# Performance work log

Hardware: AMD Instinct MI355X
Metric: run time of the kernel (lower is better)

Reference implementation:

```python
import jax, jax.numpy as jnp
import numpy as np

B, S, D, H = 4, 2048, 1024, 16
DH = D // H
SCALE = float(np.sqrt(DH))


def setup_inputs() -> dict:
    key = jax.random.key(0)
    ks = jax.random.split(key, 5)
    std = 1.0 / np.sqrt(D)
    return {
        "x": jax.random.normal(ks[0], (B, S, D), dtype=jnp.float32),
        "Wq": jax.random.normal(ks[1], (D, D), dtype=jnp.float32) * std,
        "bq": jnp.zeros((D,), dtype=jnp.float32),
        "Wk": jax.random.normal(ks[2], (D, D), dtype=jnp.float32) * std,
        "bk": jnp.zeros((D,), dtype=jnp.float32),
        "Wv": jax.random.normal(ks[3], (D, D), dtype=jnp.float32) * std,
        "bv": jnp.zeros((D,), dtype=jnp.float32),
        "Wo": jax.random.normal(ks[4], (D, D), dtype=jnp.float32) * std,
        "bo": jnp.zeros((D,), dtype=jnp.float32),
        "padding_mask": jnp.ones((B, S), dtype=jnp.int32),
    }


def reference(x, Wq, bq, Wk, bk, Wv, bv, Wo, bo, padding_mask):
    b, s, d = x.shape
    # QKV projections, split heads -> [b, h, s, dh]
    q = (x @ Wq + bq).reshape(b, s, H, DH).transpose(0, 2, 1, 3)
    k = (x @ Wk + bk).reshape(b, s, H, DH).transpose(0, 2, 1, 3)
    v = (x @ Wv + bv).reshape(b, s, H, DH).transpose(0, 2, 1, 3)
    # scaled scores [b, h, s, s]
    scores = jnp.einsum('bhqd,bhkd->bhqk', q, k) / SCALE
    neg_inf = jnp.float32(-jnp.inf)
    causal = jnp.tril(jnp.ones((s, s), dtype=bool))  # [s, s]
    scores = jnp.where(causal[None, None, :, :], scores, neg_inf)
    pad = (padding_mask != 0)[:, None, None, :]  # [b,1,1,s] on key axis
    scores = jnp.where(pad, scores, neg_inf)
    weights = jax.nn.softmax(scores, axis=-1)
    weights = jnp.nan_to_num(weights, nan=0.0)  # fully-masked rows -> 0
    # dropout is identity in eval / p=0
    attended = jnp.einsum('bhqk,bhkd->bhqd', weights, v)
    attended = attended.transpose(0, 2, 1, 3).reshape(b, s, d)
    return attended @ Wo + bo
```

## Files before the change

kernel.cpp:

```cpp
#include <hip/hip_runtime.h>
#include <hip/hip_bf16.h>

#define B_   4
#define S_   2048
#define D_   1024
#define H_   16
#define DH_  64
#define M_   (B_ * S_)

typedef __attribute__((ext_vector_type(8))) short  bfrag8;
typedef __attribute__((ext_vector_type(4))) float  facc4;
typedef unsigned short u16;
typedef unsigned long long u64;

__device__ __forceinline__ u16 f2bf(float f) {
    union { __hip_bfloat16 h; u16 u; } c;
    c.h = __float2bfloat16(f);
    return c.u;
}

__device__ __forceinline__ u16 bfr(float f) {
    unsigned b = __float_as_uint(f);
    return (u16)((b + 0x7FFFu + ((b >> 16) & 1u)) >> 16);
}

__device__ __forceinline__ void gl_lds16(const u16* g, u16* l) {
    __builtin_amdgcn_global_load_lds((const __attribute__((address_space(1))) void*)g,
                                     (__attribute__((address_space(3))) void*)l,
                                     16, 0, 0);
}

__global__ __launch_bounds__(256) void cvt_x(const float* __restrict__ x,
                                             u16* __restrict__ o, int n) {
    int i = (blockIdx.x * 256 + threadIdx.x) * 4;
    if (i >= n) return;
    float4 v = *(const float4*)(x + i);
    ushort4 r;
    r.x = f2bf(v.x); r.y = f2bf(v.y); r.z = f2bf(v.z); r.w = f2bf(v.w);
    *(ushort4*)(o + i) = r;
}

__global__ __launch_bounds__(256) void cvt_wt(const float* __restrict__ w0, const float* __restrict__ w1,
                                              const float* __restrict__ w2, const float* __restrict__ w3,
                                              u16* __restrict__ o0, u16* __restrict__ o1,
                                              u16* __restrict__ o2, u16* __restrict__ o3) {
    const float* w; u16* o;
    switch (blockIdx.z) {
        case 0: w = w0; o = o0; break;
        case 1: w = w1; o = o1; break;
        case 2: w = w2; o = o2; break;
        default: w = w3; o = o3; break;
    }
    __shared__ u16 t[32][33];
    int kb = blockIdx.x * 32, nb = blockIdx.y * 32;
    int c = threadIdx.x & 31, r0 = threadIdx.x >> 5;
#pragma unroll
    for (int i = 0; i < 4; i++) {
        int r = r0 + 8 * i;
        t[r][c] = f2bf(w[(kb + r) * D_ + nb + c]);
    }
    __syncthreads();
#pragma unroll
    for (int i = 0; i < 4; i++) {
        int r = r0 + 8 * i;
        o[(nb + r) * D_ + kb + c] = t[c][r];
    }
}

__global__ __launch_bounds__(64) void pack_pm(const int* __restrict__ pm,
                                              unsigned* __restrict__ pmw) {
    int b = blockIdx.x, lane = threadIdx.x;
#pragma unroll
    for (int j = 0; j < 32; ++j) {
        u64 m = __ballot(pm[b * S_ + j * 64 + lane] != 0);
        if (lane == 0) {
            pmw[b * 64 + 2 * j]     = (unsigned)m;
            pmw[b * 64 + 2 * j + 1] = (unsigned)(m >> 32);
        }
    }
}

#define ABUF_ (256 * 64)
#define TBUF_ ((256 + 128) * 64)

__device__ __forceinline__ void gemm_body256(const u16* __restrict__ A,
                                             const u16* __restrict__ BT,
                                             const float* __restrict__ bias,
                                             void* __restrict__ Cout, int mode, float scale,
                                             u16* S, int nb, int mb) {
    int tid = threadIdx.x;
    int w = tid >> 6, lane = tid & 63, quad = lane >> 4, l16 = lane & 15;
    int wm = (w >> 1) * 64, wn = (w & 1) * 64;
    int x7 = l16 & 7;

    const u16* Aga[4]; const u16* Bga[2];
#pragma unroll
    for (int i = 0; i < 4; ++i) {
        int idx = i * 512 + tid, row = idx >> 3;
        int lu = (idx & 7) ^ (row & 7);
        Aga[i] = A + (size_t)(mb + row) * D_ + lu * 8;
    }
#pragma unroll
    for (int i = 0; i < 2; ++i) {
        int idx = i * 512 + tid, row = idx >> 3;
        int lu = (idx & 7) ^ (row & 7);
        Bga[i] = BT + (size_t)(nb + row) * D_ + lu * 8;
    }

    facc4 acc[4][4] = {};

#pragma unroll
    for (int i = 0; i < 4; ++i) gl_lds16(Aga[i], S + (i * 512 + tid) * 8);
#pragma unroll
    for (int i = 0; i < 2; ++i) gl_lds16(Bga[i], S + ABUF_ + (i * 512 + tid) * 8);
    asm volatile("s_waitcnt vmcnt(0)" ::: "memory");
    __builtin_amdgcn_sched_barrier(0);
    __builtin_amdgcn_s_barrier();
    __builtin_amdgcn_sched_barrier(0);

    for (int kt = 0; kt < 16; ++kt) {
        u16* Cb = S + (kt & 1) * TBUF_;
        u16* Nb = S + ((kt & 1) ^ 1) * TBUF_;
        if (kt < 15) {
            int ko = (kt + 1) * 64;
#pragma unroll
            for (int i = 0; i < 4; ++i) gl_lds16(Aga[i] + ko, Nb + (i * 512 + tid) * 8);
#pragma unroll
            for (int i = 0; i < 2; ++i) gl_lds16(Bga[i] + ko, Nb + ABUF_ + (i * 512 + tid) * 8);
        }
#pragma unroll
        for (int k2 = 0; k2 < 2; ++k2) {
            int pu = ((k2 * 4 + quad) ^ x7) * 8;
            bfrag8 af[4], bf[4];
#pragma unroll
            for (int mt = 0; mt < 4; ++mt)
                af[mt] = *(const bfrag8*)(Cb + (wm + mt * 16 + l16) * 64 + pu);
#pragma unroll
            for (int nt = 0; nt < 4; ++nt)
                bf[nt] = *(const bfrag8*)(Cb + ABUF_ + (wn + nt * 16 + l16) * 64 + pu);
            __builtin_amdgcn_s_setprio(1);
#pragma unroll
            for (int mt = 0; mt < 4; ++mt)
#pragma unroll
                for (int nt = 0; nt < 4; ++nt)
                    acc[mt][nt] = __builtin_amdgcn_mfma_f32_16x16x32_bf16(af[mt], bf[nt], acc[mt][nt], 0, 0, 0);
            __builtin_amdgcn_s_setprio(0);
        }
        asm volatile("s_waitcnt vmcnt(0)" ::: "memory");
        __builtin_amdgcn_sched_barrier(0);
        __builtin_amdgcn_s_barrier();
        __builtin_amdgcn_sched_barrier(0);
    }

#pragma unroll
    for (int mt = 0; mt < 4; ++mt) {
        int m_base = mb + wm + mt * 16 + quad * 4;
#pragma unroll
        for (int nt = 0; nt < 4; ++nt) {
            int n = nb + wn + nt * 16 + l16;
            float bv = bias[n];
            int h = n >> 6, dd = n & 63;
#pragma unroll
            for (int r = 0; r < 4; ++r) {
                int m = m_base + r;
                float v = (acc[mt][nt][r] + bv) * scale;
                int bi = m >> 11, s = m & (S_ - 1);
                if (mode == 0) {
                    ((u16*)Cout)[(((bi * H_ + h) * S_) + s) * DH_ + dd] = bfr(v);
                } else if (mode == 1) {
                    ((u16*)Cout)[(((bi * H_ + h) * DH_) + dd) * S_ + s] = bfr(v);
                } else {
                    ((float*)Cout)[(size_t)m * D_ + n] = v;
                }
            }
        }
    }
}

#define CE_Q 0.18033688011112042f

__global__ __launch_bounds__(512, 2) void gemm_qkv(const u16* __restrict__ A,
                                                const u16* __restrict__ WTq, const float* __restrict__ bq, u16* __restrict__ Qb,
                                                const u16* __restrict__ WTk, const float* __restrict__ bk, u16* __restrict__ Kb,
                                                const u16* __restrict__ WTv, const float* __restrict__ bv, u16* __restrict__ VTb) {
    __shared__ __attribute__((aligned(16))) u16 Sh[2 * TBUF_];
    int lid = blockIdx.x;
    int xcd = lid & 7, s = lid >> 3;
    int z = s >> 5, inner = s & 31;
    int mb = (xcd * 4 + (inner >> 3)) * 256;
    int nb = (inner & 7) * 128;
    switch (z) {
        case 0: gemm_body256(A, WTq, bq, Qb, 0, CE_Q, Sh, nb, mb); break;
        case 1: gemm_body256(A, WTk, bk, Kb, 0, 1.0f, Sh, nb, mb); break;
        default: gemm_body256(A, WTv, bv, VTb, 1, 1.0f, Sh, nb, mb); break;
    }
}

__global__ __launch_bounds__(512, 2) void gemm_o(const u16* __restrict__ A,
                                              const u16* __restrict__ WTo, const float* __restrict__ bo,
                                              float* __restrict__ out) {
    __shared__ __attribute__((aligned(16))) u16 Sh[2 * TBUF_];
    int lid = blockIdx.x;
    int xcd = lid & 7, s = lid >> 3;
    int mb = (xcd * 4 + (s >> 3)) * 256;
    int nb = (s & 7) * 128;
    gemm_body256(A, WTo, bo, out, 2, 1.0f, Sh, nb, mb);
}

__device__ __forceinline__ void soft_pv(const float* p, float& lp, facc4* oaccq,
                                        const bfrag8* vf, int a0, int a1, bool qlo) {
    float rs = 0.f;
    unsigned pk[4];
#pragma unroll
    for (int j = 0; j < 4; ++j) {
        float e0 = exp2f(p[2 * j]);
        float e1 = exp2f(p[2 * j + 1]);
        rs += e0; rs += e1;
        pk[j] = __builtin_amdgcn_perm(__float_as_uint(e1), __float_as_uint(e0), 0x07060302u);
    }
    lp += rs;
    union { unsigned d[4]; bfrag8 v; } pb;
    {
        unsigned lo, hi;
        lo = __builtin_amdgcn_ds_bpermute(a0, (int)pk[0]);
        hi = __builtin_amdgcn_ds_bpermute(a0, (int)pk[2]);
        pb.d[0] = qlo ? lo : hi;
        lo = __builtin_amdgcn_ds_bpermute(a0, (int)pk[1]);
        hi = __builtin_amdgcn_ds_bpermute(a0, (int)pk[3]);
        pb.d[1] = qlo ? lo : hi;
        lo = __builtin_amdgcn_ds_bpermute(a1, (int)pk[0]);
        hi = __builtin_amdgcn_ds_bpermute(a1, (int)pk[2]);
        pb.d[2] = qlo ? lo : hi;
        lo = __builtin_amdgcn_ds_bpermute(a1, (int)pk[1]);
        hi = __builtin_amdgcn_ds_bpermute(a1, (int)pk[3]);
        pb.d[3] = qlo ? lo : hi;
    }
    __builtin_amdgcn_s_setprio(1);
#pragma unroll
    for (int dt = 0; dt < 4; ++dt)
        oaccq[dt] = __builtin_amdgcn_mfma_f32_16x16x32_bf16(vf[dt], pb.v, oaccq[dt], 0, 0, 0);
    __builtin_amdgcn_s_setprio(0);
}

__global__ __launch_bounds__(256, 4) void attn(const u16* __restrict__ Q,
                                               const u16* __restrict__ K,
                                               const u16* __restrict__ VT,
                                               const unsigned* __restrict__ pmw,
                                               u16* __restrict__ Aout) {
    __shared__ __attribute__((aligned(16))) u16 Ks[2][32 * 64];
    __shared__ __attribute__((aligned(16))) u16 Vs[2][64 * 32];

    int tid = threadIdx.x, w = tid >> 6, lane = tid & 63;
    int quad = lane >> 4, l16 = lane & 15;

    int lid = blockIdx.x;
    int bh  = (lid & 7) * 8 + ((lid >> 3) & 7);
    int g   = lid >> 6;
    int gq = g >> 2, gr = g & 3;
    int ci = (gq == 0) ? 15 - gr : (gq == 1) ? gr : (gq == 2) ? 11 - gr : 4 + gr;
    int b = bh >> 4, h = bh & 15;

    int qbase = ci * 128;
    int qw = qbase + w * 32;
    int tmax = (qbase >> 5) + 3;

    const u16* Qp = Q + (size_t)(b * H_ + h) * S_ * DH_;
    const u16* Kp = K + (size_t)(b * H_ + h) * S_ * DH_;
    const u16* Vp = VT + (size_t)(b * H_ + h) * DH_ * S_;
    const unsigned* pmb = pmw + b * 64;
    u16* Ao = Aout + (size_t)b * S_ * D_ + h * DH_;

    int krow = tid >> 3, ku = tid & 7;
    const u16* Kg = Kp + krow * DH_ + ((ku ^ (krow & 7)) * 8);
    int vrow = tid >> 2, vu = tid & 3;
    const u16* Vg = Vp + vrow * S_ + ((vu ^ (vrow & 3)) * 8);
    u16* Kl[2] = { &Ks[0][tid * 8], &Ks[1][tid * 8] };
    u16* Vl[2] = { &Vs[0][tid * 8], &Vs[1][tid * 8] };

    int k7 = l16 & 7, v3 = l16 & 3;

    int a0 = ((((2 * quad) & 3) * 16 + l16) << 2);
    int a1 = ((((2 * quad + 1) & 3) * 16 + l16) << 2);
    bool qlo = quad < 2;

    bfrag8 qf[2][2];
#pragma unroll
    for (int qt = 0; qt < 2; ++qt)
#pragma unroll
        for (int cc = 0; cc < 2; ++cc)
            qf[qt][cc] = *(const bfrag8*)(Qp + (qw + qt * 16 + l16) * DH_ + cc * 32 + quad * 8);

    facc4 oacc[2][4] = {};
    float lp[2] = {0.f, 0.f};

    gl_lds16(Kg, Kl[0]);
    gl_lds16(Vg, Vl[0]);
    unsigned vmn = pmb[0];
    __syncthreads();

    for (int t = 0; t <= tmax; ++t) {
        int cur = t & 1, nxt = cur ^ 1;
        unsigned vm = vmn;
        if (t < tmax) {
            int k1 = (t + 1) * 32;
            gl_lds16(Kg + k1 * DH_, Kl[nxt]);
            gl_lds16(Vg + k1, Vl[nxt]);
            vmn = pmb[t + 1];
        }
        int k0 = t * 32;
        const u16* Kc = Ks[cur];
        const u16* Vc = Vs[cur];

        bfrag8 kf00 = *(const bfrag8*)(Kc + (l16 * 8        + ((quad)     ^ k7)) * 8);
        bfrag8 kf01 = *(const bfrag8*)(Kc + (l16 * 8        + ((quad + 4) ^ k7)) * 8);
        bfrag8 kf10 = *(const bfrag8*)(Kc + ((l16 + 16) * 8 + ((quad)     ^ k7)) * 8);
        bfrag8 kf11 = *(const bfrag8*)(Kc + ((l16 + 16) * 8 + ((quad + 4) ^ k7)) * 8);
        bfrag8 vf[4];
#pragma unroll
        for (int dt = 0; dt < 4; ++dt)
            vf[dt] = *(const bfrag8*)(Vc + ((dt * 16 + l16) * 4 + (quad ^ v3)) * 8);

        facc4 st[2][2] = {};
        __builtin_amdgcn_s_setprio(1);
#pragma unroll
        for (int qt = 0; qt < 2; ++qt) {
            st[qt][0] = __builtin_amdgcn_mfma_f32_16x16x32_bf16(kf00, qf[qt][0], st[qt][0], 0, 0, 0);
            st[qt][0] = __builtin_amdgcn_mfma_f32_16x16x32_bf16(kf01, qf[qt][1], st[qt][0], 0, 0, 0);
            st[qt][1] = __builtin_amdgcn_mfma_f32_16x16x32_bf16(kf10, qf[qt][0], st[qt][1], 0, 0, 0);
            st[qt][1] = __builtin_amdgcn_mfma_f32_16x16x32_bf16(kf11, qf[qt][1], st[qt][1], 0, 0, 0);
        }
        __builtin_amdgcn_s_setprio(0);

        if (vm == 0xffffffffu && k0 + 31 < qw) {
#pragma unroll
            for (int qt = 0; qt < 2; ++qt) {
                float p[8];
#pragma unroll
                for (int kt = 0; kt < 2; ++kt)
#pragma unroll
                    for (int r = 0; r < 4; ++r) p[kt * 4 + r] = st[qt][kt][r];
                soft_pv(p, lp[qt], oacc[qt], vf, a0, a1, qlo);
            }
        } else {
#pragma unroll
            for (int qt = 0; qt < 2; ++qt) {
                int q0 = qw + qt * 16;
                float p[8];
#pragma unroll
                for (int kt = 0; kt < 2; ++kt)
#pragma unroll
                    for (int r = 0; r < 4; ++r) {
                        int kl = kt * 16 + quad * 4 + r;
                        bool ok = ((vm >> kl) & 1u) && (k0 + kl <= q0 + l16);
                        p[kt * 4 + r] = ok ? st[qt][kt][r] : -1e30f;
                    }
                soft_pv(p, lp[qt], oacc[qt], vf, a0, a1, qlo);
            }
        }
        __syncthreads();
    }

#pragma unroll
    for (int qt = 0; qt < 2; ++qt) {
        float l = lp[qt];
        l += __shfl_xor(l, 16);
        l += __shfl_xor(l, 32);
        float linv = (l > 0.f) ? 1.f / l : 0.f;
        size_t qoff = (size_t)(qw + qt * 16 + l16) * D_;
#pragma unroll
        for (int dt = 0; dt < 4; ++dt) {
            union { u16 hh[4]; u64 q; } pk4;
#pragma unroll
            for (int r = 0; r < 4; ++r) pk4.hh[r] = bfr(oacc[qt][dt][r] * linv);
            *(u64*)(Ao + qoff + dt * 16 + quad * 4) = pk4.q;
        }
    }
}

extern "C" void kernel_launch(void* const* d_in, const int* in_sizes, int n_in,
                              void* d_out, int out_size, void* d_ws, size_t ws_size,
                              hipStream_t stream) {
    const float* x  = (const float*)d_in[0];
    const float* Wq = (const float*)d_in[1];
    const float* bq = (const float*)d_in[2];
    const float* Wk = (const float*)d_in[3];
    const float* bk = (const float*)d_in[4];
    const float* Wv = (const float*)d_in[5];
    const float* bv = (const float*)d_in[6];
    const float* Wo = (const float*)d_in[7];
    const float* bo = (const float*)d_in[8];
    const int*   pm = (const int*)d_in[9];
    float* out = (float*)d_out;

    char* ws = (char*)d_ws;
    const size_t SZ_XD = (size_t)M_ * D_ * 2;
    const size_t SZ_W  = (size_t)D_ * D_ * 2;
    u16* X16 = (u16*)ws;
    u16* WTq = (u16*)(ws + SZ_XD);
    u16* WTk = (u16*)(ws + SZ_XD + SZ_W);
    u16* WTv = (u16*)(ws + SZ_XD + 2 * SZ_W);
    u16* WTo = (u16*)(ws + SZ_XD + 3 * SZ_W);
    u16* Qb  = (u16*)(ws + SZ_XD + 4 * SZ_W);
    u16* Kb  = (u16*)(ws + 2 * SZ_XD + 4 * SZ_W);
    u16* VTb = (u16*)(ws + 3 * SZ_XD + 4 * SZ_W);
    u16* Att = X16;
    unsigned* PMW = (unsigned*)WTq;

    cvt_x<<<(M_ * D_) / (256 * 4), 256, 0, stream>>>(x, X16, M_ * D_);
    cvt_wt<<<dim3(D_ / 32, D_ / 32, 4), 256, 0, stream>>>(Wq, Wk, Wv, Wo, WTq, WTk, WTv, WTo);

    gemm_qkv<<<dim3(768), 512, 0, stream>>>(X16, WTq, bq, Qb, WTk, bk, Kb, WTv, bv, VTb);

    pack_pm<<<4, 64, 0, stream>>>(pm, PMW);

    attn<<<dim3(1024), 256, 0, stream>>>(Qb, Kb, VTb, PMW, Att);

    gemm_o<<<dim3(256), 512, 0, stream>>>(Att, WTo, bo, out);
}
```

Measured before the change: 268.2 us.

## Triple-buffer GEMM loads, merge conversion kernels, fold mask packing into attention

The GEMM main loop moves from double to triple LDS buffering, prefetching two k-tiles ahead with a partial vmcnt wait so loads overlap compute for longer. The LDS footprint grows by half, so launch bounds drop to one block per CU and occupancy falls. The x and weight conversion kernels are merged into a single launch, and the padding-mask pack kernel is removed. Each attention block now ballots the mask into shared memory itself, which saves launches but repeats the mask reads in every block.

New measurement: 251.1 us. 1.07x faster.

```diff
diff --git a/kernel.cpp b/kernel.cpp
--- a/kernel.cpp
+++ b/kernel.cpp
@@ -30,58 +30,51 @@
                                      16, 0, 0);
 }
 
-__global__ __launch_bounds__(256) void cvt_x(const float* __restrict__ x,
-                                             u16* __restrict__ o, int n) {
-    int i = (blockIdx.x * 256 + threadIdx.x) * 4;
-    if (i >= n) return;
-    float4 v = *(const float4*)(x + i);
-    ushort4 r;
-    r.x = f2bf(v.x); r.y = f2bf(v.y); r.z = f2bf(v.z); r.w = f2bf(v.w);
-    *(ushort4*)(o + i) = r;
-}
-
-__global__ __launch_bounds__(256) void cvt_wt(const float* __restrict__ w0, const float* __restrict__ w1,
-                                              const float* __restrict__ w2, const float* __restrict__ w3,
-                                              u16* __restrict__ o0, u16* __restrict__ o1,
-                                              u16* __restrict__ o2, u16* __restrict__ o3) {
-    const float* w; u16* o;
-    switch (blockIdx.z) {
-        case 0: w = w0; o = o0; break;
-        case 1: w = w1; o = o1; break;
-        case 2: w = w2; o = o2; break;
-        default: w = w3; o = o3; break;
-    }
+__global__ __launch_bounds__(256) void prep(const float* __restrict__ x, u16* __restrict__ X16,
+                                            const float* __restrict__ w0, const float* __restrict__ w1,
+                                            const float* __restrict__ w2, const float* __restrict__ w3,
+                                            u16* __restrict__ o0, u16* __restrict__ o1,
+                                            u16* __restrict__ o2, u16* __restrict__ o3) {
     __shared__ u16 t[32][33];
-    int kb = blockIdx.x * 32, nb = blockIdx.y * 32;
-    int c = threadIdx.x & 31, r0 = threadIdx.x >> 5;
-#pragma unroll
-    for (int i = 0; i < 4; i++) {
-        int r = r0 + 8 * i;
-        t[r][c] = f2bf(w[(kb + r) * D_ + nb + c]);
-    }
-    __syncthreads();
-#pragma unroll
-    for (int i = 0; i < 4; i++) {
-        int r = r0 + 8 * i;
-        o[(nb + r) * D_ + kb + c] = t[c][r];
-    }
-}
-
-__global__ __launch_bounds__(64) void pack_pm(const int* __restrict__ pm,
-                                              unsigned* __restrict__ pmw) {
-    int b = blockIdx.x, lane = threadIdx.x;
-#pragma unroll
-    for (int j = 0; j < 32; ++j) {
-        u64 m = __ballot(pm[b * S_ + j * 64 + lane] != 0);
-        if (lane == 0) {
-            pmw[b * 64 + 2 * j]     = (unsigned)m;
-            pmw[b * 64 + 2 * j + 1] = (unsigned)(m >> 32);
+    int bid = blockIdx.x;
+    if (bid < 4096) {
+        int i = (bid * 256 + threadIdx.x) * 8;
+        float4 v0 = *(const float4*)(x + i);
+        float4 v1 = *(const float4*)(x + i + 4);
+        ushort4 r0, r1;
+        r0.x = f2bf(v0.x); r0.y = f2bf(v0.y); r0.z = f2bf(v0.z); r0.w = f2bf(v0.w);
+        r1.x = f2bf(v1.x); r1.y = f2bf(v1.y); r1.z = f2bf(v1.z); r1.w = f2bf(v1.w);
+        *(ushort4*)(X16 + i) = r0;
+        *(ushort4*)(X16 + i + 4) = r1;
+    } else {
+        int lid = bid - 4096;
+        int z = lid >> 10, r = lid & 1023;
+        const float* w; u16* o;
+        switch (z) {
+            case 0: w = w0; o = o0; break;
+            case 1: w = w1; o = o1; break;
+            case 2: w = w2; o = o2; break;
+            default: w = w3; o = o3; break;
+        }
+        int kb = (r >> 5) * 32, nb = (r & 31) * 32;
+        int c = threadIdx.x & 31, r0 = threadIdx.x >> 5;
+#pragma unroll
+        for (int i = 0; i < 4; i++) {
+            int rr = r0 + 8 * i;
+            t[rr][c] = f2bf(w[(kb + rr) * D_ + nb + c]);
+        }
+        __syncthreads();
+#pragma unroll
+        for (int i = 0; i < 4; i++) {
+            int rr = r0 + 8 * i;
+            o[(nb + rr) * D_ + kb + c] = t[c][rr];
         }
     }
 }
 
 #define ABUF_ (256 * 64)
 #define TBUF_ ((256 + 128) * 64)
+#define NKT_  16
 
 __device__ __forceinline__ void gemm_body256(const u16* __restrict__ A,
                                              const u16* __restrict__ BT,
@@ -109,25 +102,17 @@
 
     facc4 acc[4][4] = {};
 
-#pragma unroll
-    for (int i = 0; i < 4; ++i) gl_lds16(Aga[i], S + (i * 512 + tid) * 8);
-#pragma unroll
-    for (int i = 0; i < 2; ++i) gl_lds16(Bga[i], S + ABUF_ + (i * 512 + tid) * 8);
-    asm volatile("s_waitcnt vmcnt(0)" ::: "memory");
-    __builtin_amdgcn_sched_barrier(0);
-    __builtin_amdgcn_s_barrier();
-    __builtin_amdgcn_sched_barrier(0);
-
-    for (int kt = 0; kt < 16; ++kt) {
-        u16* Cb = S + (kt & 1) * TBUF_;
-        u16* Nb = S + ((kt & 1) ^ 1) * TBUF_;
-        if (kt < 15) {
-            int ko = (kt + 1) * 64;
-#pragma unroll
-            for (int i = 0; i < 4; ++i) gl_lds16(Aga[i] + ko, Nb + (i * 512 + tid) * 8);
-#pragma unroll
-            for (int i = 0; i < 2; ++i) gl_lds16(Bga[i] + ko, Nb + ABUF_ + (i * 512 + tid) * 8);
-        }
+    u16* Bu0 = S;
+    u16* Bu1 = S + TBUF_;
+    u16* Bu2 = S + 2 * TBUF_;
+
+    auto stage = [&](u16* Nb, int ko) {
+#pragma unroll
+        for (int i = 0; i < 4; ++i) gl_lds16(Aga[i] + ko, Nb + (i * 512 + tid) * 8);
+#pragma unroll
+        for (int i = 0; i < 2; ++i) gl_lds16(Bga[i] + ko, Nb + ABUF_ + (i * 512 + tid) * 8);
+    };
+    auto compute = [&](const u16* Cb) {
 #pragma unroll
         for (int k2 = 0; k2 < 2; ++k2) {
             int pu = ((k2 * 4 + quad) ^ x7) * 8;
@@ -146,10 +131,21 @@
                     acc[mt][nt] = __builtin_amdgcn_mfma_f32_16x16x32_bf16(af[mt], bf[nt], acc[mt][nt], 0, 0, 0);
             __builtin_amdgcn_s_setprio(0);
         }
-        asm volatile("s_waitcnt vmcnt(0)" ::: "memory");
+    };
+
+    stage(Bu0, 0);
+    stage(Bu1, 64);
+
+    u16 *bc = Bu0, *bn = Bu1, *bs = Bu2;
+    for (int kt = 0; kt < NKT_; ++kt) {
+        if (kt < NKT_ - 1) asm volatile("s_waitcnt vmcnt(6)" ::: "memory");
+        else               asm volatile("s_waitcnt vmcnt(0)" ::: "memory");
         __builtin_amdgcn_sched_barrier(0);
         __builtin_amdgcn_s_barrier();
         __builtin_amdgcn_sched_barrier(0);
+        if (kt + 2 < NKT_) stage(bs, (kt + 2) * 64);
+        compute(bc);
+        u16* tmp = bc; bc = bn; bn = bs; bs = tmp;
     }
 
 #pragma unroll
@@ -179,11 +175,11 @@
 
 #define CE_Q 0.18033688011112042f
 
-__global__ __launch_bounds__(512, 2) void gemm_qkv(const u16* __restrict__ A,
+__global__ __launch_bounds__(512, 1) void gemm_qkv(const u16* __restrict__ A,
                                                 const u16* __restrict__ WTq, const float* __restrict__ bq, u16* __restrict__ Qb,
                                                 const u16* __restrict__ WTk, const float* __restrict__ bk, u16* __restrict__ Kb,
                                                 const u16* __restrict__ WTv, const float* __restrict__ bv, u16* __restrict__ VTb) {
-    __shared__ __attribute__((aligned(16))) u16 Sh[2 * TBUF_];
+    __shared__ __attribute__((aligned(16))) u16 Sh[3 * TBUF_];
     int lid = blockIdx.x;
     int xcd = lid & 7, s = lid >> 3;
     int z = s >> 5, inner = s & 31;
@@ -196,10 +192,10 @@
     }
 }
 
-__global__ __launch_bounds__(512, 2) void gemm_o(const u16* __restrict__ A,
+__global__ __launch_bounds__(512, 1) void gemm_o(const u16* __restrict__ A,
                                               const u16* __restrict__ WTo, const float* __restrict__ bo,
                                               float* __restrict__ out) {
-    __shared__ __attribute__((aligned(16))) u16 Sh[2 * TBUF_];
+    __shared__ __attribute__((aligned(16))) u16 Sh[3 * TBUF_];
     int lid = blockIdx.x;
     int xcd = lid & 7, s = lid >> 3;
     int mb = (xcd * 4 + (s >> 3)) * 256;
@@ -245,10 +241,11 @@
 __global__ __launch_bounds__(256, 4) void attn(const u16* __restrict__ Q,
                                                const u16* __restrict__ K,
                                                const u16* __restrict__ VT,
-                                               const unsigned* __restrict__ pmw,
+                                               const int* __restrict__ pm,
                                                u16* __restrict__ Aout) {
     __shared__ __attribute__((aligned(16))) u16 Ks[2][32 * 64];
     __shared__ __attribute__((aligned(16))) u16 Vs[2][64 * 32];
+    __shared__ unsigned pms[64];
 
     int tid = threadIdx.x, w = tid >> 6, lane = tid & 63;
     int quad = lane >> 4, l16 = lane & 15;
@@ -267,8 +264,14 @@
     const u16* Qp = Q + (size_t)(b * H_ + h) * S_ * DH_;
     const u16* Kp = K + (size_t)(b * H_ + h) * S_ * DH_;
     const u16* Vp = VT + (size_t)(b * H_ + h) * DH_ * S_;
-    const unsigned* pmb = pmw + b * 64;
     u16* Ao = Aout + (size_t)b * S_ * D_ + h * DH_;
+
+#pragma unroll
+    for (int i = 0; i < 8; ++i) {
+        int j2 = w * 16 + i * 2;
+        u64 m = __ballot(pm[b * S_ + j2 * 32 + lane] != 0);
+        if (lane == 0) { pms[j2] = (unsigned)m; pms[j2 + 1] = (unsigned)(m >> 32); }
+    }
 
     int krow = tid >> 3, ku = tid & 7;
     const u16* Kg = Kp + krow * DH_ + ((ku ^ (krow & 7)) * 8);
@@ -295,8 +298,8 @@
 
     gl_lds16(Kg, Kl[0]);
     gl_lds16(Vg, Vl[0]);
-    unsigned vmn = pmb[0];
     __syncthreads();
+    unsigned vmn = pms[0];
 
     for (int t = 0; t <= tmax; ++t) {
         int cur = t & 1, nxt = cur ^ 1;
@@ -305,7 +308,7 @@
             int k1 = (t + 1) * 32;
             gl_lds16(Kg + k1 * DH_, Kl[nxt]);
             gl_lds16(Vg + k1, Vl[nxt]);
-            vmn = pmb[t + 1];
+            vmn = pms[t + 1];
         }
         int k0 = t * 32;
         const u16* Kc = Ks[cur];
@@ -404,16 +407,12 @@
     u16* Kb  = (u16*)(ws + 2 * SZ_XD + 4 * SZ_W);
     u16* VTb = (u16*)(ws + 3 * SZ_XD + 4 * SZ_W);
     u16* Att = X16;
-    unsigned* PMW = (unsigned*)WTq;
-
-    cvt_x<<<(M_ * D_) / (256 * 4), 256, 0, stream>>>(x, X16, M_ * D_);
-    cvt_wt<<<dim3(D_ / 32, D_ / 32, 4), 256, 0, stream>>>(Wq, Wk, Wv, Wo, WTq, WTk, WTv, WTo);
+
+    prep<<<dim3(8192), 256, 0, stream>>>(x, X16, Wq, Wk, Wv, Wo, WTq, WTk, WTv, WTo);
 
     gemm_qkv<<<dim3(768), 512, 0, stream>>>(X16, WTq, bq, Qb, WTk, bk, Kb, WTv, bv, VTb);
 
-    pack_pm<<<4, 64, 0, stream>>>(pm, PMW);
-
-    attn<<<dim3(1024), 256, 0, stream>>>(Qb, Kb, VTb, PMW, Att);
+    attn<<<dim3(1024), 256, 0, stream>>>(Qb, Kb, VTb, pm, Att);
 
     gemm_o<<<dim3(256), 512, 0, stream>>>(Att, WTo, bo, out);
 }
```
